# Optimization experiments

Measured on AMD Instinct MI355X. Metric: run time of the kernel, lower is better.

Reference implementation:

```python
import jax, jax.numpy as jnp
import numpy as np

BN_EPS = 1e-5


def setup_inputs() -> dict:
    key = jax.random.key(0)
    ks = jax.random.split(key, 10)
    B, C, L = 16, 512, 1024
    scale = 1.0 / np.sqrt(C)
    inp = {
        "x": jax.random.normal(ks[0], (B, C, L), dtype=jnp.float32),
        "gamma": jnp.ones((C,), jnp.float32),
        "beta": jnp.zeros((C,), jnp.float32),
        "Wq": jax.random.normal(ks[1], (C, C), jnp.float32) * scale,
        "bq": jnp.zeros((C,), jnp.float32),
        "Wk": jax.random.normal(ks[2], (C, C), jnp.float32) * scale,
        "bk": jnp.zeros((C,), jnp.float32),
        "Wv": jax.random.normal(ks[3], (C, C), jnp.float32) * scale,
        "bv": jnp.zeros((C,), jnp.float32),
        "Wp": jax.random.normal(ks[4], (C, C), jnp.float32) * scale,
        "bp": jnp.zeros((C,), jnp.float32),
    }
    return inp


def _pointwise(W, b, h):
    # Conv1d with kernel_size=1 == per-position linear: [C_out,C_in] x [B,C_in,L]
    return jnp.einsum("oc,bcl->bol", W, h) + b[None, :, None]


def reference(x, gamma, beta, Wq, bq, Wk, bk, Wv, bv, Wp, bp):
    B, C, L = x.shape
    # BatchNorm1d (training-mode batch statistics over batch & length dims)
    mean = jnp.mean(x, axis=(0, 2), keepdims=True)
    var = jnp.var(x, axis=(0, 2), keepdims=True)
    hn = (x - mean) * jax.lax.rsqrt(var + BN_EPS)
    hn = hn * gamma[None, :, None] + beta[None, :, None]

    q = _pointwise(Wq, bq, hn)  # [B,C,L]
    k = _pointwise(Wk, bk, hn)
    v = _pointwise(Wv, bv, hn)

    # attn[b,i,j] = sum_c q[b,c,i] k[b,c,j] / sqrt(C); i=query pos, j=key pos
    attn = jnp.einsum("bci,bcj->bij", q, k) * (C ** -0.5)
    attn = jax.nn.softmax(attn, axis=-1)

    # out[b,c,i] = sum_j attn[b,i,j] v[b,c,j]
    h_ = jnp.einsum("bij,bcj->bci", attn, v)
    h_ = _pointwise(Wp, bp, h_)
    return x + h_
```

## Files before the change

### kernel.cpp

```cpp
#include <hip/hip_runtime.h>
#include <hip/hip_bf16.h>


#define BB 16
#define CC 512
#define LL 1024
#define SCALE 0.04419417382415922f

typedef __bf16 bf16x8 __attribute__((ext_vector_type(8)));
typedef float  f32x4  __attribute__((ext_vector_type(4)));

__device__ inline unsigned short bf16_bits(float f) {
  __hip_bfloat16 h = __float2bfloat16(f);
  return __builtin_bit_cast(unsigned short, h);
}
__device__ inline float bits_lo(unsigned int u) {
  return __builtin_bit_cast(float, u << 16);
}
__device__ inline float bits_hi(unsigned int u) {
  return __builtin_bit_cast(float, u & 0xffff0000u);
}

__global__ __launch_bounds__(256) void bn_stats(
    const float* __restrict__ x, const float* __restrict__ gamma,
    const float* __restrict__ beta, float* __restrict__ scl,
    float* __restrict__ sft) {
  int c = blockIdx.x;
  int t = threadIdx.x;
  float s = 0.f, s2 = 0.f;
  for (int b = 0; b < BB; ++b) {
    float4 v = ((const float4*)(x + ((size_t)(b * CC + c)) * LL))[t];
    s  += v.x + v.y + v.z + v.w;
    s2 += v.x * v.x + v.y * v.y + v.z * v.z + v.w * v.w;
  }
  for (int m = 32; m; m >>= 1) { s += __shfl_xor(s, m, 64); s2 += __shfl_xor(s2, m, 64); }
  __shared__ float rs[4], rs2[4];
  int wave = t >> 6, lane = t & 63;
  if (lane == 0) { rs[wave] = s; rs2[wave] = s2; }
  __syncthreads();
  if (t == 0) {
    float S  = rs[0] + rs[1] + rs[2] + rs[3];
    float S2 = rs2[0] + rs2[1] + rs2[2] + rs2[3];
    float mean = S * (1.f / 16384.f);
    float var  = S2 * (1.f / 16384.f) - mean * mean;
    float sc = gamma[c] * rsqrtf(var + 1e-5f);
    scl[c] = sc;
    sft[c] = beta[c] - mean * sc;
  }
}

__global__ __launch_bounds__(256) void cast_t(
    const float* __restrict__ Wq, const float* __restrict__ Wk,
    const float* __restrict__ Wv, const float* __restrict__ Wp,
    const float* __restrict__ bq,
    __hip_bfloat16* __restrict__ WqT, __hip_bfloat16* __restrict__ WkT,
    __hip_bfloat16* __restrict__ Avt1, __hip_bfloat16* __restrict__ Wpb,
    float* __restrict__ g2) {
  int m = blockIdx.y;
  int t = threadIdx.x;
  if (m < 2) {
    const float* src = m == 0 ? Wq : Wk;
    __hip_bfloat16* dst = m == 0 ? WqT : WkT;
    __shared__ float tile[32][33];
    int o0 = (blockIdx.x >> 4) * 32, a0 = (blockIdx.x & 15) * 32;
#pragma unroll
    for (int i = 0; i < 4; ++i) {
      int idx = t + i * 256;
      int oo = idx >> 5, aa = idx & 31;
      tile[oo][aa] = src[(size_t)(o0 + oo) * 512 + a0 + aa];
    }
    __syncthreads();
#pragma unroll
    for (int i = 0; i < 2; ++i) {
      int idx = t + i * 256;
      int aa = idx >> 4, oo = (idx & 15) * 2;
      ushort2 o;
      o.x = bf16_bits(tile[oo][aa]);
      o.y = bf16_bits(tile[oo + 1][aa]);
      *(ushort2*)(dst + (size_t)(a0 + aa) * 512 + o0 + oo) = o;
    }
  } else if (m < 4) {
    const float* src = m == 2 ? Wv : Wp;
    __hip_bfloat16* dst = m == 2 ? Avt1 : Wpb;
    int i = blockIdx.x * 1024 + t * 4;
    float4 v = *(const float4*)(src + i);
    ushort4 o;
    o.x = bf16_bits(v.x); o.y = bf16_bits(v.y);
    o.z = bf16_bits(v.z); o.w = bf16_bits(v.w);
    *(ushort4*)(dst + i) = o;
  } else {
    if (blockIdx.x >= 2) return;
    int c = blockIdx.x * 256 + t;
    float acc = 0.f;
    for (int o = 0; o < 512; ++o) acc += Wk[(size_t)o * 512 + c] * bq[o];
    g2[c] = acc;
  }
}

__global__ __launch_bounds__(256) void norm_t(
    const float* __restrict__ x, const float* __restrict__ scl,
    const float* __restrict__ sft, __hip_bfloat16* __restrict__ hnT) {
  __shared__ float tile[32][33];
  int l0 = blockIdx.x * 32, c0 = blockIdx.y * 32, b = blockIdx.z;
  int t = threadIdx.x;
#pragma unroll
  for (int i = 0; i < 4; ++i) {
    int idx = t + i * 256;
    int cc = idx >> 5, ll = idx & 31;
    tile[cc][ll] = x[((size_t)(b * CC + c0 + cc)) * LL + l0 + ll];
  }
  __syncthreads();
#pragma unroll
  for (int i = 0; i < 2; ++i) {
    int idx = t + i * 256;
    int ll = idx >> 4, cc = (idx & 15) * 2;
    float v0 = tile[cc][ll] * scl[c0 + cc] + sft[c0 + cc];
    float v1 = tile[cc + 1][ll] * scl[c0 + cc + 1] + sft[c0 + cc + 1];
    ushort2 o; o.x = bf16_bits(v0); o.y = bf16_bits(v1);
    *(ushort2*)(hnT + ((size_t)(b * LL + l0 + ll)) * CC + c0 + cc) = o;
  }
}

__global__ __launch_bounds__(256) void w_gemv(
    const __hip_bfloat16* __restrict__ hnT, const float* __restrict__ g2,
    float* __restrict__ w) {
  int wave = threadIdx.x >> 6, lane = threadIdx.x & 63;
  size_t row = (size_t)blockIdx.x * 4 + wave;
  bf16x8 h = *(const bf16x8*)(hnT + row * 512 + lane * 8);
  const float* g = g2 + lane * 8;
  float s = 0.f;
#pragma unroll
  for (int e = 0; e < 8; ++e) s += (float)h[e] * g[e];
  for (int m = 32; m; m >>= 1) s += __shfl_xor(s, m, 64);
  if (lane == 0) w[row] = s;
}

__global__ __launch_bounds__(256) void softmax_w(
    __hip_bfloat16* __restrict__ S, const float* __restrict__ w) {
  int wave = threadIdx.x >> 6, lane = threadIdx.x & 63;
  size_t row = (size_t)blockIdx.x * 4 + wave;
  uint4* p = (uint4*)(S + row * 1024);
  uint4 r0 = p[lane * 2], r1 = p[lane * 2 + 1];
  const float4* wp = (const float4*)(w + (row >> 10) * 1024 + lane * 16);
  float4 w0 = wp[0], w1 = wp[1], w2 = wp[2], w3 = wp[3];
  float wv[16] = {w0.x, w0.y, w0.z, w0.w, w1.x, w1.y, w1.z, w1.w,
                  w2.x, w2.y, w2.z, w2.w, w3.x, w3.y, w3.z, w3.w};
  float f[16];
  unsigned int ww[8] = {r0.x, r0.y, r0.z, r0.w, r1.x, r1.y, r1.z, r1.w};
#pragma unroll
  for (int i = 0; i < 8; ++i) {
    f[2 * i] = bits_lo(ww[i]) + wv[2 * i];
    f[2 * i + 1] = bits_hi(ww[i]) + wv[2 * i + 1];
  }
  float mx = f[0];
#pragma unroll
  for (int i = 1; i < 16; ++i) mx = fmaxf(mx, f[i]);
  for (int m = 32; m; m >>= 1) mx = fmaxf(mx, __shfl_xor(mx, m, 64));
  float s = 0.f;
#pragma unroll
  for (int i = 0; i < 16; ++i) { f[i] = __expf(f[i] - mx); s += f[i]; }
  for (int m = 32; m; m >>= 1) s += __shfl_xor(s, m, 64);
  float inv = 1.f / s;
  unsigned int ow[8];
#pragma unroll
  for (int i = 0; i < 8; ++i) {
    unsigned int lo = bf16_bits(f[2 * i] * inv);
    unsigned int hi = bf16_bits(f[2 * i + 1] * inv);
    ow[i] = lo | (hi << 16);
  }
  uint4 o0 = {ow[0], ow[1], ow[2], ow[3]}, o1 = {ow[4], ow[5], ow[6], ow[7]};
  p[lane * 2] = o0; p[lane * 2 + 1] = o1;
}

__device__ inline void glds(const __hip_bfloat16* g, __hip_bfloat16* l) {
  __builtin_amdgcn_global_load_lds(
      (__attribute__((address_space(1))) void*)(void*)g,
      (__attribute__((address_space(3))) void*)l, 16, 0, 0);
}

__device__ __forceinline__ void gemm_core(
    const __hip_bfloat16* __restrict__ A, int lda,
    const __hip_bfloat16* __restrict__ B, int ldb, int K,
    __hip_bfloat16* sA, __hip_bfloat16* sB, f32x4 (&acc)[4][4]) {
  const int tid = threadIdx.x;
  const int wave = tid >> 6, lane = tid & 63;
  const int wm = (wave >> 1) * 64, wn = (wave & 1) * 64;
  const int row0 = tid >> 2;
  const int ke0 = (((tid & 3) ^ ((tid >> 3) & 3)) * 8);
  const int fr = lane & 15;
  const int q = lane >> 4;
  const int colA = ((q ^ ((fr >> 1) & 3)) * 8);
  for (int k0 = 0; k0 < K; k0 += 32) {
    __syncthreads();
#pragma unroll
    for (int it = 0; it < 2; ++it) {
      const __hip_bfloat16* ga = A + (size_t)(it * 64 + row0) * lda + (k0 + ke0);
      const __hip_bfloat16* gb = B + (size_t)(it * 64 + row0) * ldb + (k0 + ke0);
      glds(ga, sA + (it * 256 + wave * 64) * 8);
      glds(gb, sB + (it * 256 + wave * 64) * 8);
    }
    __syncthreads();
    bf16x8 af[4], bfr[4];
#pragma unroll
    for (int i = 0; i < 4; ++i) {
      af[i]  = *(const bf16x8*)(sA + (wm + i * 16 + fr) * 32 + colA);
      bfr[i] = *(const bf16x8*)(sB + (wn + i * 16 + fr) * 32 + colA);
    }
#pragma unroll
    for (int i = 0; i < 4; ++i)
#pragma unroll
      for (int j = 0; j < 4; ++j)
        acc[i][j] = __builtin_amdgcn_mfma_f32_16x16x32_bf16(af[i], bfr[j], acc[i][j], 0, 0, 0);
  }
}

template <bool BIAS>
__global__ __launch_bounds__(256, 3) void gemm_bf16t(
    const __hip_bfloat16* __restrict__ A, int lda, size_t strideA,
    const __hip_bfloat16* __restrict__ B, int ldb, size_t strideB,
    __hip_bfloat16* __restrict__ D, int ldd, size_t strideD,
    const float* __restrict__ bias, float scale, int K) {
  __shared__ __align__(16) __hip_bfloat16 sA[128 * 32];
  __shared__ __align__(16) __hip_bfloat16 sB[128 * 32];
  const int bat = blockIdx.z;
  const int m0 = blockIdx.y * 128, n0 = blockIdx.x * 128;
  f32x4 acc[4][4] = {};
  gemm_core(A + (size_t)bat * strideA + (size_t)m0 * lda, lda,
            B + (size_t)bat * strideB + (size_t)n0 * ldb, ldb, K, sA, sB, acc);
  const int lane = threadIdx.x & 63, wave = threadIdx.x >> 6;
  const int wm = (wave >> 1) * 64, wn = (wave & 1) * 64;
  const int crow = (lane >> 4) * 4, ccol = lane & 15;
  __hip_bfloat16* Db = D + (size_t)bat * strideD;
#pragma unroll
  for (int j = 0; j < 4; ++j) {
    int ng = n0 + wn + j * 16 + ccol;
    float bn = BIAS ? bias[ng] : 0.f;
#pragma unroll
    for (int i = 0; i < 4; ++i) {
      int mg = m0 + wm + i * 16 + crow;
      ushort4 o;
      o.x = bf16_bits(acc[i][j][0] * scale + bn);
      o.y = bf16_bits(acc[i][j][1] * scale + bn);
      o.z = bf16_bits(acc[i][j][2] * scale + bn);
      o.w = bf16_bits(acc[i][j][3] * scale + bn);
      *(ushort4*)(Db + (size_t)ng * ldd + mg) = o;
    }
  }
}

__global__ __launch_bounds__(256, 3) void gemm_vt1(
    const __hip_bfloat16* __restrict__ Ap, const __hip_bfloat16* __restrict__ hnT,
    __hip_bfloat16* __restrict__ vN, __hip_bfloat16* __restrict__ T1T,
    const float* __restrict__ bv) {
  __shared__ __align__(16) __hip_bfloat16 sA[128 * 32];
  __shared__ __align__(16) __hip_bfloat16 sB[128 * 32];
  const int bat = blockIdx.z;
  const int m0 = blockIdx.y * 128, n0 = blockIdx.x * 128;
  f32x4 acc[4][4] = {};
  gemm_core(Ap + (size_t)m0 * 512, 512,
            hnT + (size_t)bat * LL * CC + (size_t)n0 * 512, 512, 512, sA, sB, acc);
  const int lane = threadIdx.x & 63, wave = threadIdx.x >> 6;
  const int wm = (wave >> 1) * 64, wn = (wave & 1) * 64;
  const int crow = (lane >> 4) * 4, ccol = lane & 15;
  const int mloc0 = m0 & 511;
  if (m0 < 512) {
    __hip_bfloat16* D = vN + (size_t)bat * CC * LL;
#pragma unroll
    for (int i = 0; i < 4; ++i) {
      int mg = mloc0 + wm + i * 16 + crow;
      float bv4[4];
#pragma unroll
      for (int r = 0; r < 4; ++r) bv4[r] = bv[mg + r];
#pragma unroll
      for (int j = 0; j < 4; ++j) {
        int ng = n0 + wn + j * 16 + ccol;
#pragma unroll
        for (int r = 0; r < 4; ++r)
          D[(size_t)(mg + r) * 1024 + ng] = __float2bfloat16(acc[i][j][r] + bv4[r]);
      }
    }
  } else {
    __hip_bfloat16* D = T1T + (size_t)bat * LL * CC;
#pragma unroll
    for (int j = 0; j < 4; ++j) {
      int ng = n0 + wn + j * 16 + ccol;
#pragma unroll
      for (int i = 0; i < 4; ++i) {
        int mg = mloc0 + wm + i * 16 + crow;
        ushort4 o;
        o.x = bf16_bits(acc[i][j][0]);
        o.y = bf16_bits(acc[i][j][1]);
        o.z = bf16_bits(acc[i][j][2]);
        o.w = bf16_bits(acc[i][j][3]);
        *(ushort4*)(D + (size_t)ng * 512 + mg) = o;
      }
    }
  }
}

__global__ __launch_bounds__(256, 3) void gemm_f32t(
    const __hip_bfloat16* __restrict__ A, int lda, size_t strideA,
    const __hip_bfloat16* __restrict__ B, int ldb,
    float* __restrict__ D, int ldd, size_t strideD,
    const float* __restrict__ bias, const float* __restrict__ resid, int K) {
  __shared__ __align__(16) __hip_bfloat16 sA[128 * 32];
  __shared__ __align__(16) __hip_bfloat16 sB[128 * 32];
  const int bat = blockIdx.z;
  const int m0 = blockIdx.y * 128, n0 = blockIdx.x * 128;
  f32x4 acc[4][4] = {};
  gemm_core(A + (size_t)bat * strideA + (size_t)m0 * lda, lda,
            B + (size_t)n0 * ldb, ldb, K, sA, sB, acc);
  const int lane = threadIdx.x & 63, wave = threadIdx.x >> 6;
  const int wm = (wave >> 1) * 64, wn = (wave & 1) * 64;
  const int crow = (lane >> 4) * 4, ccol = lane & 15;
  float* Db = D + (size_t)bat * strideD;
  const float* Rb = resid + (size_t)bat * strideD;
#pragma unroll
  for (int j = 0; j < 4; ++j) {
    int ng = n0 + wn + j * 16 + ccol;
    float bn = bias[ng];
#pragma unroll
    for (int i = 0; i < 4; ++i) {
      int mg = m0 + wm + i * 16 + crow;
      float4 r = *(const float4*)(Rb + (size_t)ng * ldd + mg);
      float4 o;
      o.x = acc[i][j][0] + bn + r.x;
      o.y = acc[i][j][1] + bn + r.y;
      o.z = acc[i][j][2] + bn + r.z;
      o.w = acc[i][j][3] + bn + r.w;
      *(float4*)(Db + (size_t)ng * ldd + mg) = o;
    }
  }
}

extern "C" void kernel_launch(void* const* d_in, const int* in_sizes, int n_in,
                              void* d_out, int out_size, void* d_ws, size_t ws_size,
                              hipStream_t stream) {
  const float* x     = (const float*)d_in[0];
  const float* gamma = (const float*)d_in[1];
  const float* beta  = (const float*)d_in[2];
  const float* Wq    = (const float*)d_in[3];
  const float* bq    = (const float*)d_in[4];
  const float* Wk    = (const float*)d_in[5];
  const float* bk    = (const float*)d_in[6];
  const float* Wv    = (const float*)d_in[7];
  const float* bv    = (const float*)d_in[8];
  const float* Wp    = (const float*)d_in[9];
  const float* bp    = (const float*)d_in[10];
  float* out = (float*)d_out;
  (void)bk;

  char* ws = (char*)d_ws;
  float* scl = (float*)ws;
  float* sft = scl + 512;
  float* g2  = sft + 512;
  float* w   = g2 + 512;
  __hip_bfloat16* WqT  = (__hip_bfloat16*)(w + 16384);
  __hip_bfloat16* WkT  = WqT + 262144;
  __hip_bfloat16* Wpb  = WkT + 262144;
  __hip_bfloat16* Avt1 = Wpb + 262144;
  __hip_bfloat16* Gm   = Avt1 + 262144;
  __hip_bfloat16* hnT  = Avt1 + 524288;
  __hip_bfloat16* T1T  = hnT + 8388608;
  __hip_bfloat16* vN   = T1T + 8388608;
  __hip_bfloat16* Sb   = vN + 8388608;
  __hip_bfloat16* HT   = hnT;

  const size_t sLC = (size_t)LL * CC;
  const size_t sCL = (size_t)CC * LL;
  const size_t sLLb = (size_t)LL * LL;

  bn_stats<<<512, 256, 0, stream>>>(x, gamma, beta, scl, sft);
  cast_t<<<dim3(256, 5), 256, 0, stream>>>(Wq, Wk, Wv, Wp, bq,
                                           WqT, WkT, Avt1, Wpb, g2);
  norm_t<<<dim3(32, 16, 16), 256, 0, stream>>>(x, scl, sft, hnT);
  gemm_bf16t<false><<<dim3(4, 4, 1), 256, 0, stream>>>(
      WkT, 512, 0, WqT, 512, 0, Gm, 512, 0, nullptr, SCALE, 512);
  w_gemv<<<4096, 256, 0, stream>>>(hnT, g2, w);
  gemm_vt1<<<dim3(8, 8, 16), 256, 0, stream>>>(Avt1, hnT, vN, T1T, bv);
  gemm_bf16t<false><<<dim3(8, 8, 16), 256, 0, stream>>>(
      T1T, 512, sLC, hnT, 512, sLC, Sb, 1024, sLLb, nullptr, 1.f, 512);
  softmax_w<<<4096, 256, 0, stream>>>(Sb, w);
  gemm_bf16t<false><<<dim3(8, 4, 16), 256, 0, stream>>>(
      vN, 1024, sCL, Sb, 1024, sLLb, HT, 512, sLC, nullptr, 1.f, 1024);
  gemm_f32t<<<dim3(4, 8, 16), 256, 0, stream>>>(
      HT, 512, sLC, Wpb, 512, out, 1024, sCL, bp, x, 512);
}
```

Baseline: 273.9 us.

## Use K=64 GEMM tiles, fold weight prep into one kernel, fuse w bias into score GEMM

Replaces the K=32 shared-memory GEMM core with a K=64 version using an XOR swizzle, which halves the number of barrier pairs per tile. Merges the BN stats, weight casts, g2 GEMV and the Wq^T·Wk product into a single prep kernel, computing the small C×C product with scalar loops. This removes the transpose-cast step and a separate GEMM launch. Moves the per-key bias w into the score GEMM epilogue so softmax no longer reads it, and specializes the GEMM kernels. The larger tiles double LDS use per block, which may reduce occupancy, and the scalar 512x512x512 product in prep could become a long serial tail.

Result: faster. 260.1 us (-5.0%).

```diff
diff --git a/kernel.cpp b/kernel.cpp
--- a/kernel.cpp
+++ b/kernel.cpp
@@ -21,79 +21,61 @@
   return __builtin_bit_cast(float, u & 0xffff0000u);
 }
 
-__global__ __launch_bounds__(256) void bn_stats(
+__global__ __launch_bounds__(256) void prep(
     const float* __restrict__ x, const float* __restrict__ gamma,
-    const float* __restrict__ beta, float* __restrict__ scl,
-    float* __restrict__ sft) {
-  int c = blockIdx.x;
+    const float* __restrict__ beta, const float* __restrict__ Wq,
+    const float* __restrict__ bq, const float* __restrict__ Wk,
+    const float* __restrict__ Wv, const float* __restrict__ Wp,
+    float* __restrict__ scl, float* __restrict__ sft, float* __restrict__ g2,
+    __hip_bfloat16* __restrict__ Avt1, __hip_bfloat16* __restrict__ Wpb) {
+  int blk = blockIdx.x;
   int t = threadIdx.x;
-  float s = 0.f, s2 = 0.f;
-  for (int b = 0; b < BB; ++b) {
-    float4 v = ((const float4*)(x + ((size_t)(b * CC + c)) * LL))[t];
-    s  += v.x + v.y + v.z + v.w;
-    s2 += v.x * v.x + v.y * v.y + v.z * v.z + v.w * v.w;
-  }
-  for (int m = 32; m; m >>= 1) { s += __shfl_xor(s, m, 64); s2 += __shfl_xor(s2, m, 64); }
-  __shared__ float rs[4], rs2[4];
-  int wave = t >> 6, lane = t & 63;
-  if (lane == 0) { rs[wave] = s; rs2[wave] = s2; }
-  __syncthreads();
-  if (t == 0) {
-    float S  = rs[0] + rs[1] + rs[2] + rs[3];
-    float S2 = rs2[0] + rs2[1] + rs2[2] + rs2[3];
-    float mean = S * (1.f / 16384.f);
-    float var  = S2 * (1.f / 16384.f) - mean * mean;
-    float sc = gamma[c] * rsqrtf(var + 1e-5f);
-    scl[c] = sc;
-    sft[c] = beta[c] - mean * sc;
-  }
-}
-
-__global__ __launch_bounds__(256) void cast_t(
-    const float* __restrict__ Wq, const float* __restrict__ Wk,
-    const float* __restrict__ Wv, const float* __restrict__ Wp,
-    const float* __restrict__ bq,
-    __hip_bfloat16* __restrict__ WqT, __hip_bfloat16* __restrict__ WkT,
-    __hip_bfloat16* __restrict__ Avt1, __hip_bfloat16* __restrict__ Wpb,
-    float* __restrict__ g2) {
-  int m = blockIdx.y;
-  int t = threadIdx.x;
-  if (m < 2) {
-    const float* src = m == 0 ? Wq : Wk;
-    __hip_bfloat16* dst = m == 0 ? WqT : WkT;
-    __shared__ float tile[32][33];
-    int o0 = (blockIdx.x >> 4) * 32, a0 = (blockIdx.x & 15) * 32;
-#pragma unroll
-    for (int i = 0; i < 4; ++i) {
-      int idx = t + i * 256;
-      int oo = idx >> 5, aa = idx & 31;
-      tile[oo][aa] = src[(size_t)(o0 + oo) * 512 + a0 + aa];
-    }
+  if (blk < 512) {
+    int c = blk;
+    float s = 0.f, s2 = 0.f;
+    for (int b = 0; b < BB; ++b) {
+      float4 v = ((const float4*)(x + ((size_t)(b * CC + c)) * LL))[t];
+      s  += v.x + v.y + v.z + v.w;
+      s2 += v.x * v.x + v.y * v.y + v.z * v.z + v.w * v.w;
+    }
+    for (int m = 32; m; m >>= 1) { s += __shfl_xor(s, m, 64); s2 += __shfl_xor(s2, m, 64); }
+    __shared__ float rs[4], rs2[4];
+    int wave = t >> 6, lane = t & 63;
+    if (lane == 0) { rs[wave] = s; rs2[wave] = s2; }
     __syncthreads();
-#pragma unroll
-    for (int i = 0; i < 2; ++i) {
-      int idx = t + i * 256;
-      int aa = idx >> 4, oo = (idx & 15) * 2;
-      ushort2 o;
-      o.x = bf16_bits(tile[oo][aa]);
-      o.y = bf16_bits(tile[oo + 1][aa]);
-      *(ushort2*)(dst + (size_t)(a0 + aa) * 512 + o0 + oo) = o;
-    }
-  } else if (m < 4) {
-    const float* src = m == 2 ? Wv : Wp;
-    __hip_bfloat16* dst = m == 2 ? Avt1 : Wpb;
-    int i = blockIdx.x * 1024 + t * 4;
+    if (t == 0) {
+      float S  = rs[0] + rs[1] + rs[2] + rs[3];
+      float S2 = rs2[0] + rs2[1] + rs2[2] + rs2[3];
+      float mean = S * (1.f / 16384.f);
+      float var  = S2 * (1.f / 16384.f) - mean * mean;
+      float sc = gamma[c] * rsqrtf(var + 1e-5f);
+      scl[c] = sc;
+      sft[c] = beta[c] - mean * sc;
+    }
+  } else if (blk < 1024) {
+    const float* src = blk < 768 ? Wv : Wp;
+    __hip_bfloat16* dst = blk < 768 ? Avt1 : Wpb;
+    int i = ((blk & 255) * 256 + t) * 4;
     float4 v = *(const float4*)(src + i);
     ushort4 o;
     o.x = bf16_bits(v.x); o.y = bf16_bits(v.y);
     o.z = bf16_bits(v.z); o.w = bf16_bits(v.w);
     *(ushort4*)(dst + i) = o;
+  } else if (blk < 1026) {
+    int c = (blk - 1024) * 256 + t;
+    float acc = 0.f;
+#pragma unroll 8
+    for (int o = 0; o < 512; ++o) acc += Wk[(size_t)o * 512 + c] * bq[o];
+    g2[c] = acc * SCALE;
   } else {
-    if (blockIdx.x >= 2) return;
-    int c = blockIdx.x * 256 + t;
+    int idx = blk - 1026;
+    int a = idx >> 1;
+    int b = (idx & 1) * 256 + t;
     float acc = 0.f;
-    for (int o = 0; o < 512; ++o) acc += Wk[(size_t)o * 512 + c] * bq[o];
-    g2[c] = acc;
+#pragma unroll 8
+    for (int o = 0; o < 512; ++o)
+      acc += Wq[(size_t)o * 512 + a] * Wk[(size_t)o * 512 + b];
+    Avt1[262144 + (size_t)a * 512 + b] = __float2bfloat16(acc * SCALE);
   }
 }
 
@@ -135,23 +117,15 @@
   if (lane == 0) w[row] = s;
 }
 
-__global__ __launch_bounds__(256) void softmax_w(
-    __hip_bfloat16* __restrict__ S, const float* __restrict__ w) {
+__global__ __launch_bounds__(256) void softmax_bf16(__hip_bfloat16* __restrict__ S) {
   int wave = threadIdx.x >> 6, lane = threadIdx.x & 63;
   size_t row = (size_t)blockIdx.x * 4 + wave;
   uint4* p = (uint4*)(S + row * 1024);
   uint4 r0 = p[lane * 2], r1 = p[lane * 2 + 1];
-  const float4* wp = (const float4*)(w + (row >> 10) * 1024 + lane * 16);
-  float4 w0 = wp[0], w1 = wp[1], w2 = wp[2], w3 = wp[3];
-  float wv[16] = {w0.x, w0.y, w0.z, w0.w, w1.x, w1.y, w1.z, w1.w,
-                  w2.x, w2.y, w2.z, w2.w, w3.x, w3.y, w3.z, w3.w};
   float f[16];
   unsigned int ww[8] = {r0.x, r0.y, r0.z, r0.w, r1.x, r1.y, r1.z, r1.w};
 #pragma unroll
-  for (int i = 0; i < 8; ++i) {
-    f[2 * i] = bits_lo(ww[i]) + wv[2 * i];
-    f[2 * i + 1] = bits_hi(ww[i]) + wv[2 * i + 1];
-  }
+  for (int i = 0; i < 8; ++i) { f[2 * i] = bits_lo(ww[i]); f[2 * i + 1] = bits_hi(ww[i]); }
   float mx = f[0];
 #pragma unroll
   for (int i = 1; i < 16; ++i) mx = fmaxf(mx, f[i]);
@@ -178,72 +152,42 @@
       (__attribute__((address_space(3))) void*)l, 16, 0, 0);
 }
 
-__device__ __forceinline__ void gemm_core(
+__device__ __forceinline__ void gemm_core64(
     const __hip_bfloat16* __restrict__ A, int lda,
     const __hip_bfloat16* __restrict__ B, int ldb, int K,
     __hip_bfloat16* sA, __hip_bfloat16* sB, f32x4 (&acc)[4][4]) {
   const int tid = threadIdx.x;
   const int wave = tid >> 6, lane = tid & 63;
   const int wm = (wave >> 1) * 64, wn = (wave & 1) * 64;
-  const int row0 = tid >> 2;
-  const int ke0 = (((tid & 3) ^ ((tid >> 3) & 3)) * 8);
+  const int row0 = tid >> 3;
+  const int gchunk = ((tid & 7) ^ (row0 & 7)) * 8;
   const int fr = lane & 15;
   const int q = lane >> 4;
-  const int colA = ((q ^ ((fr >> 1) & 3)) * 8);
-  for (int k0 = 0; k0 < K; k0 += 32) {
+  for (int k0 = 0; k0 < K; k0 += 64) {
     __syncthreads();
 #pragma unroll
-    for (int it = 0; it < 2; ++it) {
-      const __hip_bfloat16* ga = A + (size_t)(it * 64 + row0) * lda + (k0 + ke0);
-      const __hip_bfloat16* gb = B + (size_t)(it * 64 + row0) * ldb + (k0 + ke0);
-      glds(ga, sA + (it * 256 + wave * 64) * 8);
-      glds(gb, sB + (it * 256 + wave * 64) * 8);
+    for (int it = 0; it < 4; ++it) {
+      const __hip_bfloat16* ga = A + (size_t)(it * 32 + row0) * lda + k0 + gchunk;
+      const __hip_bfloat16* gb = B + (size_t)(it * 32 + row0) * ldb + k0 + gchunk;
+      glds(ga, sA + it * 2048 + tid * 8);
+      glds(gb, sB + it * 2048 + tid * 8);
     }
     __syncthreads();
-    bf16x8 af[4], bfr[4];
-#pragma unroll
-    for (int i = 0; i < 4; ++i) {
-      af[i]  = *(const bf16x8*)(sA + (wm + i * 16 + fr) * 32 + colA);
-      bfr[i] = *(const bf16x8*)(sB + (wn + i * 16 + fr) * 32 + colA);
-    }
-#pragma unroll
-    for (int i = 0; i < 4; ++i)
-#pragma unroll
-      for (int j = 0; j < 4; ++j)
-        acc[i][j] = __builtin_amdgcn_mfma_f32_16x16x32_bf16(af[i], bfr[j], acc[i][j], 0, 0, 0);
-  }
-}
-
-template <bool BIAS>
-__global__ __launch_bounds__(256, 3) void gemm_bf16t(
-    const __hip_bfloat16* __restrict__ A, int lda, size_t strideA,
-    const __hip_bfloat16* __restrict__ B, int ldb, size_t strideB,
-    __hip_bfloat16* __restrict__ D, int ldd, size_t strideD,
-    const float* __restrict__ bias, float scale, int K) {
-  __shared__ __align__(16) __hip_bfloat16 sA[128 * 32];
-  __shared__ __align__(16) __hip_bfloat16 sB[128 * 32];
-  const int bat = blockIdx.z;
-  const int m0 = blockIdx.y * 128, n0 = blockIdx.x * 128;
-  f32x4 acc[4][4] = {};
-  gemm_core(A + (size_t)bat * strideA + (size_t)m0 * lda, lda,
-            B + (size_t)bat * strideB + (size_t)n0 * ldb, ldb, K, sA, sB, acc);
-  const int lane = threadIdx.x & 63, wave = threadIdx.x >> 6;
-  const int wm = (wave >> 1) * 64, wn = (wave & 1) * 64;
-  const int crow = (lane >> 4) * 4, ccol = lane & 15;
-  __hip_bfloat16* Db = D + (size_t)bat * strideD;
-#pragma unroll
-  for (int j = 0; j < 4; ++j) {
-    int ng = n0 + wn + j * 16 + ccol;
-    float bn = BIAS ? bias[ng] : 0.f;
-#pragma unroll
-    for (int i = 0; i < 4; ++i) {
-      int mg = m0 + wm + i * 16 + crow;
-      ushort4 o;
-      o.x = bf16_bits(acc[i][j][0] * scale + bn);
-      o.y = bf16_bits(acc[i][j][1] * scale + bn);
-      o.z = bf16_bits(acc[i][j][2] * scale + bn);
-      o.w = bf16_bits(acc[i][j][3] * scale + bn);
-      *(ushort4*)(Db + (size_t)ng * ldd + mg) = o;
+#pragma unroll
+    for (int s = 0; s < 2; ++s) {
+      bf16x8 af[4], bfr[4];
+#pragma unroll
+      for (int i = 0; i < 4; ++i) {
+        int ra = wm + i * 16 + fr;
+        af[i] = *(const bf16x8*)(sA + ra * 64 + (((s * 4 + q) ^ (fr & 7)) * 8));
+        int rb = wn + i * 16 + fr;
+        bfr[i] = *(const bf16x8*)(sB + rb * 64 + (((s * 4 + q) ^ (fr & 7)) * 8));
+      }
+#pragma unroll
+      for (int i = 0; i < 4; ++i)
+#pragma unroll
+        for (int j = 0; j < 4; ++j)
+          acc[i][j] = __builtin_amdgcn_mfma_f32_16x16x32_bf16(af[i], bfr[j], acc[i][j], 0, 0, 0);
     }
   }
 }
@@ -252,13 +196,13 @@
     const __hip_bfloat16* __restrict__ Ap, const __hip_bfloat16* __restrict__ hnT,
     __hip_bfloat16* __restrict__ vN, __hip_bfloat16* __restrict__ T1T,
     const float* __restrict__ bv) {
-  __shared__ __align__(16) __hip_bfloat16 sA[128 * 32];
-  __shared__ __align__(16) __hip_bfloat16 sB[128 * 32];
+  __shared__ __align__(16) __hip_bfloat16 sA[128 * 64];
+  __shared__ __align__(16) __hip_bfloat16 sB[128 * 64];
   const int bat = blockIdx.z;
   const int m0 = blockIdx.y * 128, n0 = blockIdx.x * 128;
   f32x4 acc[4][4] = {};
-  gemm_core(Ap + (size_t)m0 * 512, 512,
-            hnT + (size_t)bat * LL * CC + (size_t)n0 * 512, 512, 512, sA, sB, acc);
+  gemm_core64(Ap + (size_t)m0 * 512, 512,
+              hnT + (size_t)bat * LL * CC + (size_t)n0 * 512, 512, 512, sA, sB, acc);
   const int lane = threadIdx.x & 63, wave = threadIdx.x >> 6;
   const int wm = (wave >> 1) * 64, wn = (wave & 1) * 64;
   const int crow = (lane >> 4) * 4, ccol = lane & 15;
@@ -298,23 +242,85 @@
   }
 }
 
-__global__ __launch_bounds__(256, 3) void gemm_f32t(
-    const __hip_bfloat16* __restrict__ A, int lda, size_t strideA,
-    const __hip_bfloat16* __restrict__ B, int ldb,
-    float* __restrict__ D, int ldd, size_t strideD,
-    const float* __restrict__ bias, const float* __restrict__ resid, int K) {
-  __shared__ __align__(16) __hip_bfloat16 sA[128 * 32];
-  __shared__ __align__(16) __hip_bfloat16 sB[128 * 32];
+__global__ __launch_bounds__(256, 3) void gemm_sw(
+    const __hip_bfloat16* __restrict__ T1T, const __hip_bfloat16* __restrict__ hnT,
+    __hip_bfloat16* __restrict__ Sb, const float* __restrict__ w) {
+  __shared__ __align__(16) __hip_bfloat16 sA[128 * 64];
+  __shared__ __align__(16) __hip_bfloat16 sB[128 * 64];
+  const int bat = blockIdx.z;
+  const int m0 = blockIdx.y * 128, n0 = blockIdx.x * 128;
+  const size_t sLC = (size_t)LL * CC;
+  f32x4 acc[4][4] = {};
+  gemm_core64(T1T + (size_t)bat * sLC + (size_t)m0 * 512, 512,
+              hnT + (size_t)bat * sLC + (size_t)n0 * 512, 512, 512, sA, sB, acc);
+  const int lane = threadIdx.x & 63, wave = threadIdx.x >> 6;
+  const int wm = (wave >> 1) * 64, wn = (wave & 1) * 64;
+  const int crow = (lane >> 4) * 4, ccol = lane & 15;
+  __hip_bfloat16* Db = Sb + (size_t)bat * LL * LL;
+  const float* wb = w + (size_t)bat * LL;
+#pragma unroll
+  for (int j = 0; j < 4; ++j) {
+    int ng = n0 + wn + j * 16 + ccol;
+#pragma unroll
+    for (int i = 0; i < 4; ++i) {
+      int mg = m0 + wm + i * 16 + crow;
+      float4 wv4 = *(const float4*)(wb + mg);
+      ushort4 o;
+      o.x = bf16_bits(acc[i][j][0] + wv4.x);
+      o.y = bf16_bits(acc[i][j][1] + wv4.y);
+      o.z = bf16_bits(acc[i][j][2] + wv4.z);
+      o.w = bf16_bits(acc[i][j][3] + wv4.w);
+      *(ushort4*)(Db + (size_t)ng * 1024 + mg) = o;
+    }
+  }
+}
+
+__global__ __launch_bounds__(256, 3) void gemm_pv(
+    const __hip_bfloat16* __restrict__ vN, const __hip_bfloat16* __restrict__ Sb,
+    __hip_bfloat16* __restrict__ HT) {
+  __shared__ __align__(16) __hip_bfloat16 sA[128 * 64];
+  __shared__ __align__(16) __hip_bfloat16 sB[128 * 64];
   const int bat = blockIdx.z;
   const int m0 = blockIdx.y * 128, n0 = blockIdx.x * 128;
   f32x4 acc[4][4] = {};
-  gemm_core(A + (size_t)bat * strideA + (size_t)m0 * lda, lda,
-            B + (size_t)n0 * ldb, ldb, K, sA, sB, acc);
+  gemm_core64(vN + (size_t)bat * CC * LL + (size_t)m0 * 1024, 1024,
+              Sb + (size_t)bat * LL * LL + (size_t)n0 * 1024, 1024, 1024, sA, sB, acc);
   const int lane = threadIdx.x & 63, wave = threadIdx.x >> 6;
   const int wm = (wave >> 1) * 64, wn = (wave & 1) * 64;
   const int crow = (lane >> 4) * 4, ccol = lane & 15;
-  float* Db = D + (size_t)bat * strideD;
-  const float* Rb = resid + (size_t)bat * strideD;
+  __hip_bfloat16* Db = HT + (size_t)bat * LL * CC;
+#pragma unroll
+  for (int j = 0; j < 4; ++j) {
+    int ng = n0 + wn + j * 16 + ccol;
+#pragma unroll
+    for (int i = 0; i < 4; ++i) {
+      int mg = m0 + wm + i * 16 + crow;
+      ushort4 o;
+      o.x = bf16_bits(acc[i][j][0]);
+      o.y = bf16_bits(acc[i][j][1]);
+      o.z = bf16_bits(acc[i][j][2]);
+      o.w = bf16_bits(acc[i][j][3]);
+      *(ushort4*)(Db + (size_t)ng * 512 + mg) = o;
+    }
+  }
+}
+
+__global__ __launch_bounds__(256, 3) void gemm_f32t(
+    const __hip_bfloat16* __restrict__ HT, const __hip_bfloat16* __restrict__ Wpb,
+    float* __restrict__ D, const float* __restrict__ bias,
+    const float* __restrict__ resid) {
+  __shared__ __align__(16) __hip_bfloat16 sA[128 * 64];
+  __shared__ __align__(16) __hip_bfloat16 sB[128 * 64];
+  const int bat = blockIdx.z;
+  const int m0 = blockIdx.y * 128, n0 = blockIdx.x * 128;
+  f32x4 acc[4][4] = {};
+  gemm_core64(HT + (size_t)bat * LL * CC + (size_t)m0 * 512, 512,
+              Wpb + (size_t)n0 * 512, 512, 512, sA, sB, acc);
+  const int lane = threadIdx.x & 63, wave = threadIdx.x >> 6;
+  const int wm = (wave >> 1) * 64, wn = (wave & 1) * 64;
+  const int crow = (lane >> 4) * 4, ccol = lane & 15;
+  float* Db = D + (size_t)bat * CC * LL;
+  const float* Rb = resid + (size_t)bat * CC * LL;
 #pragma unroll
   for (int j = 0; j < 4; ++j) {
     int ng = n0 + wn + j * 16 + ccol;
@@ -322,13 +328,13 @@
 #pragma unroll
     for (int i = 0; i < 4; ++i) {
       int mg = m0 + wm + i * 16 + crow;
-      float4 r = *(const float4*)(Rb + (size_t)ng * ldd + mg);
+      float4 r = *(const float4*)(Rb + (size_t)ng * 1024 + mg);
       float4 o;
       o.x = acc[i][j][0] + bn + r.x;
       o.y = acc[i][j][1] + bn + r.y;
       o.z = acc[i][j][2] + bn + r.z;
       o.w = acc[i][j][3] + bn + r.w;
-      *(float4*)(Db + (size_t)ng * ldd + mg) = o;
+      *(float4*)(Db + (size_t)ng * 1024 + mg) = o;
     }
   }
 }
@@ -354,35 +360,22 @@
   float* scl = (float*)ws;
   float* sft = scl + 512;
   float* g2  = sft + 512;
-  float* w   = g2 + 512;
-  __hip_bfloat16* WqT  = (__hip_bfloat16*)(w + 16384);
-  __hip_bfloat16* WkT  = WqT + 262144;
-  __hip_bfloat16* Wpb  = WkT + 262144;
-  __hip_bfloat16* Avt1 = Wpb + 262144;
-  __hip_bfloat16* Gm   = Avt1 + 262144;
-  __hip_bfloat16* hnT  = Avt1 + 524288;
+  float* w   = g2 + 1024;
+  __hip_bfloat16* Avt1 = (__hip_bfloat16*)(w + 16384);
+  __hip_bfloat16* Wpb  = Avt1 + 524288;
+  __hip_bfloat16* hnT  = Wpb + 262144;
   __hip_bfloat16* T1T  = hnT + 8388608;
   __hip_bfloat16* vN   = T1T + 8388608;
   __hip_bfloat16* Sb   = vN + 8388608;
   __hip_bfloat16* HT   = hnT;
 
-  const size_t sLC = (size_t)LL * CC;
-  const size_t sCL = (size_t)CC * LL;
-  const size_t sLLb = (size_t)LL * LL;
-
-  bn_stats<<<512, 256, 0, stream>>>(x, gamma, beta, scl, sft);
-  cast_t<<<dim3(256, 5), 256, 0, stream>>>(Wq, Wk, Wv, Wp, bq,
-                                           WqT, WkT, Avt1, Wpb, g2);
+  prep<<<2050, 256, 0, stream>>>(x, gamma, beta, Wq, bq, Wk, Wv, Wp,
+                                 scl, sft, g2, Avt1, Wpb);
   norm_t<<<dim3(32, 16, 16), 256, 0, stream>>>(x, scl, sft, hnT);
-  gemm_bf16t<false><<<dim3(4, 4, 1), 256, 0, stream>>>(
-      WkT, 512, 0, WqT, 512, 0, Gm, 512, 0, nullptr, SCALE, 512);
   w_gemv<<<4096, 256, 0, stream>>>(hnT, g2, w);
   gemm_vt1<<<dim3(8, 8, 16), 256, 0, stream>>>(Avt1, hnT, vN, T1T, bv);
-  gemm_bf16t<false><<<dim3(8, 8, 16), 256, 0, stream>>>(
-      T1T, 512, sLC, hnT, 512, sLC, Sb, 1024, sLLb, nullptr, 1.f, 512);
-  softmax_w<<<4096, 256, 0, stream>>>(Sb, w);
-  gemm_bf16t<false><<<dim3(8, 4, 16), 256, 0, stream>>>(
-      vN, 1024, sCL, Sb, 1024, sLLb, HT, 512, sLC, nullptr, 1.f, 1024);
-  gemm_f32t<<<dim3(4, 8, 16), 256, 0, stream>>>(
-      HT, 512, sLC, Wpb, 512, out, 1024, sCL, bp, x, 512);
-}
+  gemm_sw<<<dim3(8, 8, 16), 256, 0, stream>>>(T1T, hnT, Sb, w);
+  softmax_bf16<<<4096, 256, 0, stream>>>(Sb);
+  gemm_pv<<<dim3(8, 4, 16), 256, 0, stream>>>(vN, Sb, HT);
+  gemm_f32t<<<dim3(4, 8, 16), 256, 0, stream>>>(HT, Wpb, out, bp, x);
+}
```
